# Kernel tuning notes

Measured on AMD Instinct MI355X. Metric: run time of the kernel, lower is better.

## Reference

```python
import jax, jax.numpy as jnp
import numpy as np

B, S, D = 1, 2048, 2048
H, KV, HD = 32, 8, 64
POWER = 100000.0


def _rotary(x):
    # x: [B, h, S, HD]; faithful to RotaryEncoder: freqs = pos / div_term
    rot_dim = HD // 2
    pos = jnp.arange(S, dtype=x.dtype)
    div = POWER ** (jnp.arange(0, HD, 2, dtype=x.dtype) / HD)  # [HD//2]
    freqs = pos[:, None] / div  # [S, HD//2]
    cos, sin = jnp.cos(freqs), jnp.sin(freqs)
    x_rot, x_pass = x[..., :rot_dim], x[..., rot_dim:]
    h = rot_dim // 2
    rot_half = jnp.concatenate([-x_rot[..., h:], x_rot[..., :h]], axis=-1)
    return jnp.concatenate([x_rot * cos + rot_half * sin, x_pass], axis=-1)


def setup_inputs() -> dict:
    key = jax.random.key(0)
    k1, k2, k3 = jax.random.split(key, 3)
    hidden_states = jax.random.normal(k1, (B, S, D), dtype=jnp.float32)
    op_size = H * HD + 2 * KV * HD
    Wqkv = jax.random.normal(k2, (D, op_size), dtype=jnp.float32) * 0.02
    Wo = jax.random.normal(k3, (H * HD, D), dtype=jnp.float32) * 0.02
    causal = jnp.tril(jnp.ones((S, S), dtype=bool))
    attention_mask = jnp.where(causal, 0.0, -1e9).astype(jnp.float32)[None, None]
    return {"hidden_states": hidden_states, "attention_mask": attention_mask,
            "Wqkv": Wqkv, "Wo": Wo}


def reference(hidden_states, attention_mask, Wqkv, Wo):
    groups = H // KV
    qkv = hidden_states @ Wqkv  # [B, S, op_size]
    qpos = H * HD
    q = qkv[..., :qpos].reshape(B, S, H, HD).transpose(0, 2, 1, 3)
    k = qkv[..., qpos:qpos + KV * HD].reshape(B, S, KV, HD).transpose(0, 2, 1, 3)
    v = qkv[..., qpos + KV * HD:].reshape(B, S, KV, HD).transpose(0, 2, 1, 3)
    q = _rotary(q)
    k = _rotary(k)
    k = jnp.repeat(k, groups, axis=1)  # GQA repeat_interleave -> [B, H, S, HD]
    v = jnp.repeat(v, groups, axis=1)
    scores = jnp.einsum('bhqd,bhkd->bhqk', q, k) / jnp.sqrt(jnp.float32(HD))
    scores = scores + attention_mask[..., :S]
    attn = jax.nn.softmax(scores.astype(jnp.float32), axis=-1).astype(v.dtype)
    out = jnp.einsum('bhqk,bhkd->bhqd', attn, v)
    out = out.transpose(0, 2, 1, 3).reshape(B, S, H * HD)
    return out @ Wo
```

## Files before the change

### kernel.cpp

```cpp
#include <hip/hip_runtime.h>
#include <hip/hip_bf16.h>
#include <cstdint>
#include <cstddef>

#define S_LEN 2048
#define D_MODEL 2048
#define NH 32
#define NKV 8
#define HDIM 64
#define OPSZ 3072
#define KOFF 2048
#define VOFF 2560

typedef float    floatx4 __attribute__((ext_vector_type(4)));
typedef __bf16   bf16x8  __attribute__((ext_vector_type(8)));
typedef __bf16   bf16x4  __attribute__((ext_vector_type(4)));
typedef __bf16   bf16_t;
typedef _Float16 f16_t;
typedef _Float16 f16x4   __attribute__((ext_vector_type(4)));

__device__ __forceinline__ void gld16(const void* g, void* l) {
  __builtin_amdgcn_global_load_lds((__attribute__((address_space(1))) void*)(void*)g,
                                   (__attribute__((address_space(3))) void*)l,
                                   16, 0, 0);
}

__global__ __launch_bounds__(256) void convert_x(const float* __restrict__ X,
                                                 bf16_t* __restrict__ Xb) {
  const int i = (blockIdx.x * 256 + threadIdx.x) * 4;
  const float4 v = *(const float4*)(X + i);
  bf16x4 t;
  t[0] = (bf16_t)v.x; t[1] = (bf16_t)v.y; t[2] = (bf16_t)v.z; t[3] = (bf16_t)v.w;
  *(bf16x4*)(Xb + i) = t;
}

__global__ __launch_bounds__(256) void transpose_w(const float* __restrict__ W,
                                                   bf16_t* __restrict__ Wt,
                                                   int K, int N) {
  __shared__ float tile[32][33];
  const int n0 = blockIdx.x * 32, k0 = blockIdx.y * 32;
  const int tx = threadIdx.x & 31, ty = threadIdx.x >> 5;
#pragma unroll
  for (int i = 0; i < 32; i += 8)
    tile[ty + i][tx] = W[(size_t)(k0 + ty + i) * N + n0 + tx];
  __syncthreads();
#pragma unroll
  for (int i = 0; i < 32; i += 8)
    Wt[(size_t)(n0 + ty + i) * K + k0 + tx] = (bf16_t)tile[tx][ty + i];
}

#define GEMM64_CORE(A_, Bt_, K_, m0_, n0_)                                        \
  const int tid = threadIdx.x;                                                    \
  const int wave = tid >> 6;                                                      \
  const int lane = tid & 63;                                                      \
  const int lane15 = lane & 15;                                                   \
  const int quad = lane >> 4;                                                     \
  const int wm = (wave & 1) * 32;                                                 \
  const int wn = (wave >> 1) * 64;                                                \
  floatx4 acc[2][4];                                                              \
  _Pragma("unroll") for (int i = 0; i < 2; i++)                                   \
    _Pragma("unroll") for (int j = 0; j < 4; j++)                                 \
      acc[i][j] = floatx4{0.f, 0.f, 0.f, 0.f};                                    \
  {                                                                               \
                                                  \
    const int ca0 = tid, ca1 = tid + 256;                                         \
    const int apan0 = ca0 >> 8, ar0 = (ca0 & 255) >> 2, ac0 = (ca0 & 3) * 8;      \
    const int apan1 = ca1 >> 8, ar1 = (ca1 & 255) >> 2, ac1 = (ca1 & 3) * 8;      \
                  \
    int bpan[4], br[4], bc[4];                                                    \
    _Pragma("unroll") for (int i = 0; i < 4; i++) {                               \
      const int c = tid + i * 256;                                                \
      bpan[i] = c >> 9; br[i] = (c & 511) >> 2; bc[i] = (c & 3) * 8;              \
    }                                                                             \
    bf16_t* lA0 = &As[(wave * 64) * 8];                                           \
    bf16_t* lA1 = &As[(256 + wave * 64) * 8];                                     \
    for (int k0 = 0; k0 < (K_); k0 += 64) {                                       \
      __syncthreads();                                                            \
      gld16((A_) + (size_t)((m0_) + ar0) * (K_) + k0 + apan0 * 32 + ac0, lA0);    \
      gld16((A_) + (size_t)((m0_) + ar1) * (K_) + k0 + apan1 * 32 + ac1, lA1);    \
      _Pragma("unroll") for (int i = 0; i < 4; i++)                               \
        gld16((Bt_) + (size_t)((n0_) + br[i]) * (K_) + k0 + bpan[i] * 32 + bc[i], \
              &Bs[(i * 256 + wave * 64) * 8]);                                    \
      __syncthreads();                                                            \
      _Pragma("unroll") for (int kt = 0; kt < 2; kt++) {                          \
        bf16x8 af[2], bfr[4];                                                     \
        _Pragma("unroll") for (int mi = 0; mi < 2; mi++)                          \
          af[mi] = *(const bf16x8*)&As[kt * 2048 + (wm + mi * 16 + lane15) * 32 + quad * 8]; \
        _Pragma("unroll") for (int ni = 0; ni < 4; ni++)                          \
          bfr[ni] = *(const bf16x8*)&Bs[kt * 4096 + (wn + ni * 16 + lane15) * 32 + quad * 8]; \
        _Pragma("unroll") for (int mi = 0; mi < 2; mi++)                          \
          _Pragma("unroll") for (int ni = 0; ni < 4; ni++)                        \
            acc[mi][ni] = __builtin_amdgcn_mfma_f32_16x16x32_bf16(af[mi], bfr[ni],\
                                                                  acc[mi][ni], 0, 0, 0); \
      }                                                                           \
    }                                                                             \
  }

#define QSCALE 0.18033688011112042f
__global__ __launch_bounds__(256, 2)
void gemm_qkv_rope(const bf16_t* __restrict__ A, const bf16_t* __restrict__ Bt,
                   bf16_t* __restrict__ Qr, bf16_t* __restrict__ Kr,
                   f16_t* __restrict__ VtG) {
  __shared__ bf16_t As[2 * 64 * 32];
  __shared__ bf16_t Bs[2 * 128 * 32];
  const int m0 = blockIdx.y * 64;
  const int n0 = blockIdx.x * 128;
  GEMM64_CORE(A, Bt, D_MODEL, m0, n0)

  const int colbase = n0 + wn;
  const int s0 = m0 + wm;

  if (colbase < VOFF) {
    const bool isQ = (colbase < KOFF);
    const float k2 = 0.51905126483f;
    const float pj0 = exp2f(-(float)lane15 * k2);
    const float pj1 = pj0 * 0.0031622776601684f;
    bf16_t* dst = isQ ? (Qr + ((size_t)(colbase >> 6) * S_LEN) * HDIM)
                      : (Kr + ((size_t)((colbase - KOFF) >> 6) * S_LEN) * HDIM);
    const float qs = isQ ? QSCALE : 1.0f;
#pragma unroll
    for (int mi = 0; mi < 2; mi++) {
#pragma unroll
      for (int r = 0; r < 4; r++) {
        const int s = s0 + mi * 16 + quad * 4 + r;
        const float sf = (float)s;
        float s0s, s0c, s1s, s1c;
        __sincosf(sf * pj0, &s0s, &s0c);
        __sincosf(sf * pj1, &s1s, &s1c);
        const float x0 = acc[mi][0][r], x1 = acc[mi][1][r];
        bf16_t* row = dst + (size_t)s * HDIM + lane15;
        row[0]  = (bf16_t)((x0 * s0c - x1 * s0s) * qs);
        row[16] = (bf16_t)((x1 * s1c + x0 * s1s) * qs);
        row[32] = (bf16_t)(acc[mi][2][r] * qs);
        row[48] = (bf16_t)(acc[mi][3][r] * qs);
      }
    }
  } else {
    const int kvv = (colbase - VOFF) >> 6;
    f16_t* dst = VtG + (size_t)kvv * HDIM * S_LEN;
#pragma unroll
    for (int mi = 0; mi < 2; mi++) {
      const int s = s0 + mi * 16 + quad * 4;
#pragma unroll
      for (int ni = 0; ni < 4; ni++) {
        const int d = ni * 16 + lane15;
        f16x4 tv;
#pragma unroll
        for (int r = 0; r < 4; r++) tv[r] = (f16_t)acc[mi][ni][r];
        *(f16x4*)&dst[(size_t)d * S_LEN + s] = tv;
      }
    }
  }
}

__global__ __launch_bounds__(256, 2)
void gemm_bt_f32out(const bf16_t* __restrict__ A, const bf16_t* __restrict__ Bt,
                    float* __restrict__ C, int M, int N, int K) {
  __shared__ bf16_t As[2 * 64 * 32];
  __shared__ bf16_t Bs[2 * 128 * 32];
  const int m0 = blockIdx.y * 64;
  const int n0 = blockIdx.x * 128;
  GEMM64_CORE(A, Bt, K, m0, n0)

#pragma unroll
  for (int mi = 0; mi < 2; mi++)
#pragma unroll
    for (int r = 0; r < 4; r++) {
      const int row = m0 + wm + mi * 16 + quad * 4 + r;
#pragma unroll
      for (int ni = 0; ni < 4; ni++) {
        const int col = n0 + wn + ni * 16 + lane15;
        C[(size_t)row * N + col] = acc[mi][ni][r];
      }
    }
}

#define KST 72
#define VST 68
__global__ __launch_bounds__(256, 4)
void flash_kernel(const bf16_t* __restrict__ Qr, const bf16_t* __restrict__ Kr,
                  const f16_t* __restrict__ VtG, bf16_t* __restrict__ attn) {
  __shared__ bf16_t Ks[2][64 * KST];
  __shared__ f16_t  Vt[2][64 * VST];

  const int tid = threadIdx.x;
  const int wave = tid >> 6;
  const int lane = tid & 63;
  const int lane15 = lane & 15;
  const int quad = lane >> 4;
  const int bx = blockIdx.x;
  const int h = bx & 31;
  const int qblk = 31 - (bx >> 5);
  const int q0 = qblk * 64;
  const int rq = q0 + wave * 16;
  const int kv = h >> 2;
  const size_t kbase = (size_t)kv * S_LEN * HDIM;
  const size_t vbase = (size_t)kv * HDIM * S_LEN;

  const int kr_ = tid >> 3, kc_ = (tid & 7) * 8;
  const int vd_ = tid >> 4, vc_ = (tid & 15) * 4;

  bf16x8 aq[2];
#pragma unroll
  for (int kt = 0; kt < 2; kt++)
    aq[kt] = *(const bf16x8*)&Qr[((size_t)h * S_LEN + rq + lane15) * HDIM + kt * 32 + quad * 8];

  float m_run = -1e30f, l_run = 0.f;
  floatx4 o[4];
#pragma unroll
  for (int dt = 0; dt < 4; dt++) o[dt] = floatx4{0.f, 0.f, 0.f, 0.f};

  const int nk = qblk + 1;

#pragma unroll
  for (int i = 0; i < 2; i++) {
    const int r = kr_ + i * 32;
    *(bf16x8*)&Ks[0][r * KST + kc_] = *(const bf16x8*)&Kr[kbase + (size_t)r * HDIM + kc_];
  }
#pragma unroll
  for (int i = 0; i < 4; i++) {
    const int d = vd_ + i * 16;
    *(f16x4*)&Vt[0][d * VST + vc_] = *(const f16x4*)&VtG[vbase + (size_t)d * S_LEN + vc_];
  }

  for (int t = 0; t < nk; ++t) {
    const int p0 = t * 64;
    const int cur = t & 1;
    __syncthreads();

    if (t + 1 < nk) {
      const int nxt = cur ^ 1;
      const int pn = p0 + 64;
#pragma unroll
      for (int i = 0; i < 2; i++) {
        const int r = kr_ + i * 32;
        *(bf16x8*)&Ks[nxt][r * KST + kc_] = *(const bf16x8*)&Kr[kbase + (size_t)(pn + r) * HDIM + kc_];
      }
#pragma unroll
      for (int i = 0; i < 4; i++) {
        const int d = vd_ + i * 16;
        *(f16x4*)&Vt[nxt][d * VST + vc_] = *(const f16x4*)&VtG[vbase + (size_t)d * S_LEN + pn + vc_];
      }
    }

    floatx4 sc[4];
#pragma unroll
    for (int nt = 0; nt < 4; nt++) sc[nt] = floatx4{0.f, 0.f, 0.f, 0.f};
#pragma unroll
    for (int kt = 0; kt < 2; kt++) {
      bf16x8 ak[4];
#pragma unroll
      for (int nt = 0; nt < 4; nt++)
        ak[nt] = *(const bf16x8*)&Ks[cur][(nt * 16 + lane15) * KST + kt * 32 + quad * 8];
#pragma unroll
      for (int nt = 0; nt < 4; nt++)
        sc[nt] = __builtin_amdgcn_mfma_f32_16x16x32_bf16(ak[nt], aq[kt], sc[nt], 0, 0, 0);
    }

    if (p0 + 63 > rq) {
#pragma unroll
      for (int nt = 0; nt < 4; nt++)
#pragma unroll
        for (int r = 0; r < 4; r++) {
          const int kpos = p0 + nt * 16 + quad * 4 + r;
          const int qrow = rq + lane15;
          if (kpos > qrow) sc[nt][r] = -1e30f;
        }
    }

    float mt = fmaxf(fmaxf(sc[0][0], sc[0][1]), fmaxf(sc[0][2], sc[0][3]));
#pragma unroll
    for (int nt = 1; nt < 4; nt++)
#pragma unroll
      for (int r = 0; r < 4; r++) mt = fmaxf(mt, sc[nt][r]);
    mt = fmaxf(mt, __shfl_xor(mt, 16));
    mt = fmaxf(mt, __shfl_xor(mt, 32));
    const float mnew = fmaxf(m_run, mt);
    const float alpha = exp2f(m_run - mnew);
    m_run = mnew;
    float rs = 0.f;
    f16x4 ph[4];
#pragma unroll
    for (int nt = 0; nt < 4; nt++) {
      f16x4 pv;
#pragma unroll
      for (int r = 0; r < 4; r++) {
        const float p = exp2f(sc[nt][r] - mnew);
        rs += p;
        pv[r] = (f16_t)p;
      }
      ph[nt] = pv;
    }
    rs += __shfl_xor(rs, 16);
    rs += __shfl_xor(rs, 32);
    l_run = l_run * alpha + rs;
#pragma unroll
    for (int dt = 0; dt < 4; dt++)
#pragma unroll
      for (int r = 0; r < 4; r++) o[dt][r] *= alpha;

#pragma unroll
    for (int kt4 = 0; kt4 < 4; kt4++) {
      f16x4 av[4];
#pragma unroll
      for (int dt = 0; dt < 4; dt++)
        av[dt] = *(const f16x4*)&Vt[cur][(dt * 16 + lane15) * VST + kt4 * 16 + quad * 4];
#pragma unroll
      for (int dt = 0; dt < 4; dt++)
        o[dt] = __builtin_amdgcn_mfma_f32_16x16x16f16(av[dt], ph[kt4], o[dt], 0, 0, 0);
    }
  }

  const float inv = 1.0f / l_run;
  const int s = rq + lane15;
#pragma unroll
  for (int dt = 0; dt < 4; dt++) {
    bf16x4 tv;
#pragma unroll
    for (int r = 0; r < 4; r++) tv[r] = (bf16_t)(o[dt][r] * inv);
    *(bf16x4*)&attn[(size_t)s * D_MODEL + h * HDIM + dt * 16 + quad * 4] = tv;
  }
}

extern "C" void kernel_launch(void* const* d_in, const int* in_sizes, int n_in,
                              void* d_out, int out_size, void* d_ws, size_t ws_size,
                              hipStream_t stream) {
  (void)in_sizes; (void)n_in; (void)out_size; (void)ws_size;
  const float* hidden = (const float*)d_in[0];
  const float* Wqkv = (const float*)d_in[2];
  const float* Wo   = (const float*)d_in[3];
  float* out = (float*)d_out;

  char* ws = (char*)d_ws;
  size_t off = 0;
  auto alloc = [&](size_t bytes) -> void* {
    void* p = ws + off;
    off += (bytes + 255) & ~(size_t)255;
    return p;
  };
  bf16_t* Xb    = (bf16_t*)alloc((size_t)S_LEN * D_MODEL * 2);
  bf16_t* WqkvT = (bf16_t*)alloc((size_t)OPSZ * D_MODEL * 2);
  bf16_t* WoT   = (bf16_t*)alloc((size_t)D_MODEL * D_MODEL * 2);
  bf16_t* Qr    = (bf16_t*)alloc((size_t)NH * S_LEN * HDIM * 2);
  bf16_t* Kr    = (bf16_t*)alloc((size_t)NKV * S_LEN * HDIM * 2);
  f16_t*  VtG   = (f16_t*) alloc((size_t)NKV * HDIM * S_LEN * 2);
  bf16_t* attn  = (bf16_t*)alloc((size_t)S_LEN * D_MODEL * 2);

  convert_x<<<(S_LEN * D_MODEL) / 1024, 256, 0, stream>>>(hidden, Xb);
  transpose_w<<<dim3(OPSZ / 32, D_MODEL / 32), 256, 0, stream>>>(Wqkv, WqkvT, D_MODEL, OPSZ);
  transpose_w<<<dim3(D_MODEL / 32, D_MODEL / 32), 256, 0, stream>>>(Wo, WoT, D_MODEL, D_MODEL);
  gemm_qkv_rope<<<dim3(OPSZ / 128, S_LEN / 64), 256, 0, stream>>>(Xb, WqkvT, Qr, Kr, VtG);
  flash_kernel<<<dim3(32 * NH), 256, 0, stream>>>(Qr, Kr, VtG, attn);
  gemm_bt_f32out<<<dim3(D_MODEL / 128, S_LEN / 64), 256, 0, stream>>>(attn, WoT, out, S_LEN, D_MODEL, D_MODEL);
}
```

Measured before the change: 223.9 us.

## Merge prep kernels, widen flash KV tile to 128 single-buffered, raise GEMM occupancy

Fuses the X conversion and both weight transposes into one prep launch to cut launch overhead. The flash kernel now processes 128 keys per iteration with a single LDS buffer and explicit syncs, replacing the 64-key double-buffered prefetch. This halves the loop count and barriers but drops the load/compute overlap, and for even qblk the last tile covers fully masked keys. The GEMM launch bounds go from 2 to 3 blocks per CU, which may restrict registers.

```diff
diff --git a/kernel.cpp b/kernel.cpp
--- a/kernel.cpp
+++ b/kernel.cpp
@@ -18,6 +18,7 @@
 typedef __bf16   bf16_t;
 typedef _Float16 f16_t;
 typedef _Float16 f16x4   __attribute__((ext_vector_type(4)));
+typedef _Float16 f16x8   __attribute__((ext_vector_type(8)));
 
 __device__ __forceinline__ void gld16(const void* g, void* l) {
   __builtin_amdgcn_global_load_lds((__attribute__((address_space(1))) void*)(void*)g,
@@ -25,28 +26,33 @@
                                    16, 0, 0);
 }
 
-__global__ __launch_bounds__(256) void convert_x(const float* __restrict__ X,
-                                                 bf16_t* __restrict__ Xb) {
-  const int i = (blockIdx.x * 256 + threadIdx.x) * 4;
-  const float4 v = *(const float4*)(X + i);
-  bf16x4 t;
-  t[0] = (bf16_t)v.x; t[1] = (bf16_t)v.y; t[2] = (bf16_t)v.z; t[3] = (bf16_t)v.w;
-  *(bf16x4*)(Xb + i) = t;
-}
-
-__global__ __launch_bounds__(256) void transpose_w(const float* __restrict__ W,
-                                                   bf16_t* __restrict__ Wt,
-                                                   int K, int N) {
-  __shared__ float tile[32][33];
-  const int n0 = blockIdx.x * 32, k0 = blockIdx.y * 32;
+__global__ __launch_bounds__(256)
+void prep_kernel(const float* __restrict__ X, const float* __restrict__ Wqkv,
+                 const float* __restrict__ Wo, bf16_t* __restrict__ Xb,
+                 bf16_t* __restrict__ WqkvT, bf16_t* __restrict__ WoT) {
+  const int bx = blockIdx.x;
+  const int k0 = blockIdx.y * 32;
   const int tx = threadIdx.x & 31, ty = threadIdx.x >> 5;
-#pragma unroll
-  for (int i = 0; i < 32; i += 8)
-    tile[ty + i][tx] = W[(size_t)(k0 + ty + i) * N + n0 + tx];
-  __syncthreads();
-#pragma unroll
-  for (int i = 0; i < 32; i += 8)
-    Wt[(size_t)(n0 + ty + i) * K + k0 + tx] = (bf16_t)tile[tx][ty + i];
+  if (bx < 160) {
+    __shared__ float tile[32][33];
+    const float* W; bf16_t* Wt; int N, n0;
+    if (bx < 96) { W = Wqkv; Wt = WqkvT; N = OPSZ;    n0 = bx * 32; }
+    else         { W = Wo;   Wt = WoT;   N = D_MODEL; n0 = (bx - 96) * 32; }
+#pragma unroll
+    for (int i = 0; i < 32; i += 8)
+      tile[ty + i][tx] = W[(size_t)(k0 + ty + i) * N + n0 + tx];
+    __syncthreads();
+#pragma unroll
+    for (int i = 0; i < 32; i += 8)
+      Wt[(size_t)(n0 + ty + i) * D_MODEL + k0 + tx] = (bf16_t)tile[tx][ty + i];
+  } else {
+    const int n0 = (bx - 160) * 32;
+#pragma unroll
+    for (int i = 0; i < 32; i += 8) {
+      const size_t idx = (size_t)(k0 + ty + i) * D_MODEL + n0 + tx;
+      Xb[idx] = (bf16_t)X[idx];
+    }
+  }
 }
 
 #define GEMM64_CORE(A_, Bt_, K_, m0_, n0_)                                        \
@@ -97,7 +103,7 @@
   }
 
 #define QSCALE 0.18033688011112042f
-__global__ __launch_bounds__(256, 2)
+__global__ __launch_bounds__(256, 3)
 void gemm_qkv_rope(const bf16_t* __restrict__ A, const bf16_t* __restrict__ Bt,
                    bf16_t* __restrict__ Qr, bf16_t* __restrict__ Kr,
                    f16_t* __restrict__ VtG) {
@@ -153,7 +159,7 @@
   }
 }
 
-__global__ __launch_bounds__(256, 2)
+__global__ __launch_bounds__(256, 3)
 void gemm_bt_f32out(const bf16_t* __restrict__ A, const bf16_t* __restrict__ Bt,
                     float* __restrict__ C, int M, int N, int K) {
   __shared__ bf16_t As[2 * 64 * 32];
@@ -176,12 +182,12 @@
 }
 
 #define KST 72
-#define VST 68
+#define VST 136
 __global__ __launch_bounds__(256, 4)
 void flash_kernel(const bf16_t* __restrict__ Qr, const bf16_t* __restrict__ Kr,
                   const f16_t* __restrict__ VtG, bf16_t* __restrict__ attn) {
-  __shared__ bf16_t Ks[2][64 * KST];
-  __shared__ f16_t  Vt[2][64 * VST];
+  __shared__ bf16_t Ks[128 * KST];
+  __shared__ f16_t  Vt[64 * VST];
 
   const int tid = threadIdx.x;
   const int wave = tid >> 6;
@@ -198,7 +204,7 @@
   const size_t vbase = (size_t)kv * HDIM * S_LEN;
 
   const int kr_ = tid >> 3, kc_ = (tid & 7) * 8;
-  const int vd_ = tid >> 4, vc_ = (tid & 15) * 4;
+  const int vd_ = tid >> 4, vc_ = (tid & 15) * 8;
 
   bf16x8 aq[2];
 #pragma unroll
@@ -210,56 +216,38 @@
 #pragma unroll
   for (int dt = 0; dt < 4; dt++) o[dt] = floatx4{0.f, 0.f, 0.f, 0.f};
 
-  const int nk = qblk + 1;
-
-#pragma unroll
-  for (int i = 0; i < 2; i++) {
-    const int r = kr_ + i * 32;
-    *(bf16x8*)&Ks[0][r * KST + kc_] = *(const bf16x8*)&Kr[kbase + (size_t)r * HDIM + kc_];
-  }
-#pragma unroll
-  for (int i = 0; i < 4; i++) {
-    const int d = vd_ + i * 16;
-    *(f16x4*)&Vt[0][d * VST + vc_] = *(const f16x4*)&VtG[vbase + (size_t)d * S_LEN + vc_];
-  }
+  const int nk = (qblk + 2) >> 1;
 
   for (int t = 0; t < nk; ++t) {
-    const int p0 = t * 64;
-    const int cur = t & 1;
+    const int p0 = t * 128;
     __syncthreads();
-
-    if (t + 1 < nk) {
-      const int nxt = cur ^ 1;
-      const int pn = p0 + 64;
-#pragma unroll
-      for (int i = 0; i < 2; i++) {
-        const int r = kr_ + i * 32;
-        *(bf16x8*)&Ks[nxt][r * KST + kc_] = *(const bf16x8*)&Kr[kbase + (size_t)(pn + r) * HDIM + kc_];
-      }
-#pragma unroll
-      for (int i = 0; i < 4; i++) {
-        const int d = vd_ + i * 16;
-        *(f16x4*)&Vt[nxt][d * VST + vc_] = *(const f16x4*)&VtG[vbase + (size_t)d * S_LEN + pn + vc_];
-      }
-    }
-
-    floatx4 sc[4];
-#pragma unroll
-    for (int nt = 0; nt < 4; nt++) sc[nt] = floatx4{0.f, 0.f, 0.f, 0.f};
+#pragma unroll
+    for (int i = 0; i < 4; i++) {
+      const int r = kr_ + i * 32;
+      *(bf16x8*)&Ks[r * KST + kc_] = *(const bf16x8*)&Kr[kbase + (size_t)(p0 + r) * HDIM + kc_];
+    }
+#pragma unroll
+    for (int i = 0; i < 4; i++) {
+      const int d = vd_ + i * 16;
+      *(f16x8*)&Vt[d * VST + vc_] = *(const f16x8*)&VtG[vbase + (size_t)d * S_LEN + p0 + vc_];
+    }
+    __syncthreads();
+
+    floatx4 sc[8];
+#pragma unroll
+    for (int nt = 0; nt < 8; nt++) sc[nt] = floatx4{0.f, 0.f, 0.f, 0.f};
 #pragma unroll
     for (int kt = 0; kt < 2; kt++) {
-      bf16x8 ak[4];
-#pragma unroll
-      for (int nt = 0; nt < 4; nt++)
-        ak[nt] = *(const bf16x8*)&Ks[cur][(nt * 16 + lane15) * KST + kt * 32 + quad * 8];
-#pragma unroll
-      for (int nt = 0; nt < 4; nt++)
-        sc[nt] = __builtin_amdgcn_mfma_f32_16x16x32_bf16(ak[nt], aq[kt], sc[nt], 0, 0, 0);
-    }
-
-    if (p0 + 63 > rq) {
-#pragma unroll
-      for (int nt = 0; nt < 4; nt++)
+#pragma unroll
+      for (int nt = 0; nt < 8; nt++) {
+        const bf16x8 ak = *(const bf16x8*)&Ks[(nt * 16 + lane15) * KST + kt * 32 + quad * 8];
+        sc[nt] = __builtin_amdgcn_mfma_f32_16x16x32_bf16(ak, aq[kt], sc[nt], 0, 0, 0);
+      }
+    }
+
+    if (p0 + 127 > rq) {
+#pragma unroll
+      for (int nt = 0; nt < 8; nt++)
 #pragma unroll
         for (int r = 0; r < 4; r++) {
           const int kpos = p0 + nt * 16 + quad * 4 + r;
@@ -270,7 +258,7 @@
 
     float mt = fmaxf(fmaxf(sc[0][0], sc[0][1]), fmaxf(sc[0][2], sc[0][3]));
 #pragma unroll
-    for (int nt = 1; nt < 4; nt++)
+    for (int nt = 1; nt < 8; nt++)
 #pragma unroll
       for (int r = 0; r < 4; r++) mt = fmaxf(mt, sc[nt][r]);
     mt = fmaxf(mt, __shfl_xor(mt, 16));
@@ -279,9 +267,9 @@
     const float alpha = exp2f(m_run - mnew);
     m_run = mnew;
     float rs = 0.f;
-    f16x4 ph[4];
-#pragma unroll
-    for (int nt = 0; nt < 4; nt++) {
+    f16x4 ph[8];
+#pragma unroll
+    for (int nt = 0; nt < 8; nt++) {
       f16x4 pv;
 #pragma unroll
       for (int r = 0; r < 4; r++) {
@@ -300,14 +288,12 @@
       for (int r = 0; r < 4; r++) o[dt][r] *= alpha;
 
 #pragma unroll
-    for (int kt4 = 0; kt4 < 4; kt4++) {
-      f16x4 av[4];
-#pragma unroll
-      for (int dt = 0; dt < 4; dt++)
-        av[dt] = *(const f16x4*)&Vt[cur][(dt * 16 + lane15) * VST + kt4 * 16 + quad * 4];
-#pragma unroll
-      for (int dt = 0; dt < 4; dt++)
-        o[dt] = __builtin_amdgcn_mfma_f32_16x16x16f16(av[dt], ph[kt4], o[dt], 0, 0, 0);
+    for (int kt4 = 0; kt4 < 8; kt4++) {
+#pragma unroll
+      for (int dt = 0; dt < 4; dt++) {
+        const f16x4 av = *(const f16x4*)&Vt[(dt * 16 + lane15) * VST + kt4 * 16 + quad * 4];
+        o[dt] = __builtin_amdgcn_mfma_f32_16x16x16f16(av, ph[kt4], o[dt], 0, 0, 0);
+      }
     }
   }
 
@@ -346,9 +332,7 @@
   f16_t*  VtG   = (f16_t*) alloc((size_t)NKV * HDIM * S_LEN * 2);
   bf16_t* attn  = (bf16_t*)alloc((size_t)S_LEN * D_MODEL * 2);
 
-  convert_x<<<(S_LEN * D_MODEL) / 1024, 256, 0, stream>>>(hidden, Xb);
-  transpose_w<<<dim3(OPSZ / 32, D_MODEL / 32), 256, 0, stream>>>(Wqkv, WqkvT, D_MODEL, OPSZ);
-  transpose_w<<<dim3(D_MODEL / 32, D_MODEL / 32), 256, 0, stream>>>(Wo, WoT, D_MODEL, D_MODEL);
+  prep_kernel<<<dim3(224, 64), 256, 0, stream>>>(hidden, Wqkv, Wo, Xb, WqkvT, WoT);
   gemm_qkv_rope<<<dim3(OPSZ / 128, S_LEN / 64), 256, 0, stream>>>(Xb, WqkvT, Qr, Kr, VtG);
   flash_kernel<<<dim3(32 * NH), 256, 0, stream>>>(Qr, Kr, VtG, attn);
   gemm_bt_f32out<<<dim3(D_MODEL / 128, S_LEN / 64), 256, 0, stream>>>(attn, WoT, out, S_LEN, D_MODEL, D_MODEL);
```

Result: no change. 219.9 us (-1.8%).
